# Kernel optimization log

Hardware: AMD Instinct MI355X
Metric: run time of the kernel (lower is better)

The kernel has to match this reference:

```python
import jax, jax.numpy as jnp
import numpy as np

N = 16384

def setup_inputs() -> dict:
    key = jax.random.key(0)
    k1, k2 = jax.random.split(key)
    inputs = jax.random.normal(k1, (N,), dtype=jnp.float32)
    targets = jax.random.randint(k2, (N,), 0, 2)  # int, values in {0,1}
    return {"inputs": inputs, "targets": targets}

def reference(inputs, targets):
    # Flatten, split logits into positives (targets==1) and negatives (targets==0).
    x = inputs.reshape(-1)
    t = targets.reshape(-1).astype(jnp.float32)
    pos_mask = (t == 1.0).astype(x.dtype)  # (N,)
    neg_mask = (t == 0.0).astype(x.dtype)  # (N,)
    # BCE-with-logits against target=1 on diff = x_i - x_j is softplus(-diff).
    # Masked full NxN formulation (jit-friendly, same math as pos/neg outer diff).
    diff = x[:, None] - x[None, :]                      # (N, N)
    pair_w = pos_mask[:, None] * neg_mask[None, :]      # 1 for (pos, neg) pairs
    loss_sum = jnp.sum(jax.nn.softplus(-diff) * pair_w)
    n_pairs = jnp.sum(pair_w)
    # Original returns 0.0 if no pos or no neg examples.
    return jnp.where(n_pairs > 0, loss_sum / jnp.maximum(n_pairs, 1.0), 0.0)
```

## Files before the change

### kernel.cpp

```cpp
#include <hip/hip_runtime.h>


#define CB   1024
#define PT2  512
#define RB   16
#define NW   (PT2 / 64)

__global__ __launch_bounds__(CB)
void compact_kernel(const float* __restrict__ x, const int* __restrict__ tg,
                    int n, float* __restrict__ pos_emp, float* __restrict__ neg_en,
                    int* __restrict__ cnts) {
    __shared__ float sbuf[16384];
    __shared__ int swsum[16], swoff[16], stot;
    const int tid  = threadIdx.x;
    const int lane = tid & 63, wid = tid >> 6;
    const int n4 = n >> 2;

    float4 vf[4]; int4 vt[4];
    int lp = 0, ln = 0;
#pragma unroll
    for (int k = 0; k < 4; ++k) {
        const int i4 = tid + k * CB;
        if (i4 < n4) { vf[k] = ((const float4*)x)[i4]; vt[k] = ((const int4*)tg)[i4]; }
        else         { vf[k] = make_float4(0,0,0,0); vt[k] = make_int4(-1,-1,-1,-1); }
        lp += (vt[k].x==1) + (vt[k].y==1) + (vt[k].z==1) + (vt[k].w==1);
        ln += (vt[k].x==0) + (vt[k].y==0) + (vt[k].z==0) + (vt[k].w==0);
    }

    const int c = lp | (ln << 16);
    int inc = c;
#pragma unroll
    for (int off = 1; off < 64; off <<= 1) {
        int u = __shfl_up(inc, off, 64);
        if (lane >= off) inc += u;
    }
    if (lane == 63) swsum[wid] = inc;
    __syncthreads();
    if (tid < 16) {
        int val = swsum[tid];
        int sc = val;
#pragma unroll
        for (int off = 1; off < 16; off <<= 1) {
            int u = __shfl_up(sc, off, 64);
            if (tid >= off) sc += u;
        }
        swoff[tid] = sc - val;
        if (tid == 15) stot = sc;
    }
    __syncthreads();
    const int ex = swoff[wid] + (inc - c);
    int op = ex & 0xffff;
    int on = ex >> 16;
#pragma unroll
    for (int k = 0; k < 4; ++k) {
        const float vx[4] = {vf[k].x, vf[k].y, vf[k].z, vf[k].w};
        const int   tx[4] = {vt[k].x, vt[k].y, vt[k].z, vt[k].w};
#pragma unroll
        for (int j = 0; j < 4; ++j) {
            if (tx[j] == 1)      sbuf[op++]           = __expf(-vx[j]);
            else if (tx[j] == 0) sbuf[n - 1 - (on++)] = __expf(vx[j]);
        }
    }
    __syncthreads();
    const int np = stot & 0xffff;
    const int nn = stot >> 16;
    const int nn_pad = (nn + 3) & ~3;
    for (int i = tid; i < np; i += CB)          pos_emp[i] = sbuf[i];
    for (int i = tid; i < nn; i += CB)          neg_en[i]  = sbuf[n - 1 - i];
    for (int i = nn + tid; i < nn_pad; i += CB) neg_en[i]  = 0.f;
    if (tid == 0) { cnts[0] = np; cnts[1] = nn; cnts[2] = nn_pad; }
}

__global__ __launch_bounds__(PT2)
void pair_kernel(const float* __restrict__ pos_emp, const float* __restrict__ neg_en,
                 const int* __restrict__ cnts, double* __restrict__ wpart) {
    const int bid = blockIdx.x, tid = threadIdx.x;
    const int wid = tid >> 6, lane = tid & 63;
    const int gw  = bid * NW + wid;
    const int np = cnts[0];
    const int nnpad4 = cnts[2] >> 2;
    const int rbase = bid * RB;

    if (rbase >= np || nnpad4 == 0) {
        if (lane == 0) wpart[gw] = 0.0;
        return;
    }

    float emp[RB];
#pragma unroll
    for (int r = 0; r < RB; ++r) {
        const int row = rbase + r;
        emp[r] = (row < np) ? pos_emp[row] : 0.f;
    }

    float acc0 = 0.f, acc1 = 0.f;
#define TERM(EN, R)  __builtin_fmaf((EN), emp[R], 1.0f)
#define Q4(EN, R0)   (((TERM(EN,R0) * TERM(EN,(R0)+1)) * TERM(EN,(R0)+2)) * TERM(EN,(R0)+3))
#define DO_COL(EN)                                      \
    do {                                                \
        const float en_ = (EN);                         \
        acc0 += __log2f(Q4(en_, 0) * Q4(en_, 4));       \
        acc1 += __log2f(Q4(en_, 8) * Q4(en_, 12));      \
    } while (0)

    const float4* __restrict__ en4 = (const float4*)neg_en;
#pragma unroll 2
    for (int v4 = tid; v4 < nnpad4; v4 += PT2) {
        const float4 e4 = en4[v4];
        DO_COL(e4.x);
        DO_COL(e4.y);
        DO_COL(e4.z);
        DO_COL(e4.w);
    }
#undef DO_COL
#undef Q4
#undef TERM

    float s = acc0 + acc1;
#pragma unroll
    for (int off = 32; off > 0; off >>= 1) s += __shfl_down(s, off, 64);
    if (lane == 0) wpart[gw] = (double)s;
}

__global__ __launch_bounds__(1024)
void finalize_kernel(const int* __restrict__ cnts, const double* __restrict__ wpart,
                     int nwaves, float* __restrict__ out) {
    const int tid = threadIdx.x;
    double d = 0.0;
    for (int k = tid; k < nwaves; k += 1024) d += wpart[k];
#pragma unroll
    for (int off = 32; off > 0; off >>= 1) d += __shfl_down(d, off, 64);
    __shared__ double fsum[16];
    if ((tid & 63) == 0) fsum[tid >> 6] = d;
    __syncthreads();
    if (tid == 0) {
        double s = 0.0;
#pragma unroll
        for (int w = 0; w < 16; ++w) s += fsum[w];
        const double npairs = (double)cnts[0] * (double)cnts[1];
        out[0] = (npairs > 0.0) ? (float)(s * 0.6931471805599453 / npairs) : 0.0f;
    }
}

extern "C" void kernel_launch(void* const* d_in, const int* in_sizes, int n_in,
                              void* d_out, int out_size, void* d_ws, size_t ws_size,
                              hipStream_t stream) {
    const float* x  = (const float*)d_in[0];
    const int*   tg = (const int*)d_in[1];
    const int n = in_sizes[0];

    char* ws = (char*)d_ws;
    float*  pos_emp = (float*)(ws);
    float*  neg_en  = (float*)(ws + 65536);
    int*    cnts    = (int*)(ws + 135168);
    double* wpart   = (double*)(ws + 139264);

    const int nblocks = (n + RB - 1) / RB;
    const int nwaves  = nblocks * NW;
    compact_kernel<<<1, CB, 0, stream>>>(x, tg, n, pos_emp, neg_en, cnts);
    pair_kernel<<<nblocks, PT2, 0, stream>>>(pos_emp, neg_en, cnts, wpart);
    finalize_kernel<<<1, 1024, 0, stream>>>(cnts, wpart, nwaves, (float*)d_out);
}
```

Measured before the change: 21.66 us.

## Parallelize compaction across 64 blocks with per-block prefix recount and ballot scatter

```diff
diff --git a/kernel.cpp b/kernel.cpp
--- a/kernel.cpp
+++ b/kernel.cpp
@@ -1,74 +1,74 @@
 #include <hip/hip_runtime.h>
 
 
-#define CB   1024
+#define K1B  64
+#define K1T  256
 #define PT2  512
 #define RB   16
 #define NW   (PT2 / 64)
 
-__global__ __launch_bounds__(CB)
-void compact_kernel(const float* __restrict__ x, const int* __restrict__ tg,
-                    int n, float* __restrict__ pos_emp, float* __restrict__ neg_en,
-                    int* __restrict__ cnts) {
-    __shared__ float sbuf[16384];
-    __shared__ int swsum[16], swoff[16], stot;
-    const int tid  = threadIdx.x;
-    const int lane = tid & 63, wid = tid >> 6;
-    const int n4 = n >> 2;
+__global__ __launch_bounds__(K1T)
+void pcompact(const float* __restrict__ x, const int* __restrict__ tg, int n,
+              float* __restrict__ pos_emp, float* __restrict__ neg_en,
+              int* __restrict__ cnts) {
+    __shared__ int wred[K1T / 64], wvc[K1T / 64], base_s, tots;
+    const int b = blockIdx.x, t = threadIdx.x;
+    const int lane = t & 63, w = t >> 6;
+    const int s0 = b * K1T;
 
-    float4 vf[4]; int4 vt[4];
-    int lp = 0, ln = 0;
+    int cp = 0, cn = 0;
+    const int4* t4 = (const int4*)tg;
+    for (int v = t; v < (s0 >> 2); v += K1T) {
+        const int4 tv = t4[v];
+        cp += (tv.x == 1) + (tv.y == 1) + (tv.z == 1) + (tv.w == 1);
+        cn += (tv.x == 0) + (tv.y == 0) + (tv.z == 0) + (tv.w == 0);
+    }
+    int pk = cp | (cn << 16);
 #pragma unroll
-    for (int k = 0; k < 4; ++k) {
-        const int i4 = tid + k * CB;
-        if (i4 < n4) { vf[k] = ((const float4*)x)[i4]; vt[k] = ((const int4*)tg)[i4]; }
-        else         { vf[k] = make_float4(0,0,0,0); vt[k] = make_int4(-1,-1,-1,-1); }
-        lp += (vt[k].x==1) + (vt[k].y==1) + (vt[k].z==1) + (vt[k].w==1);
-        ln += (vt[k].x==0) + (vt[k].y==0) + (vt[k].z==0) + (vt[k].w==0);
+    for (int off = 32; off > 0; off >>= 1) pk += __shfl_down(pk, off, 64);
+    if (lane == 0) wred[w] = pk;
+    __syncthreads();
+    if (t == 0) {
+        int s = 0;
+#pragma unroll
+        for (int i = 0; i < K1T / 64; ++i) s += wred[i];
+        base_s = s;
     }
 
-    const int c = lp | (ln << 16);
-    int inc = c;
+    const int e = s0 + t;
+    const int   tv = (e < n) ? tg[e] : -1;
+    const float xv = (e < n) ? x[e] : 0.f;
+    const int isp = (tv == 1), isn = (tv == 0);
+    const unsigned long long mp = __ballot(isp);
+    const unsigned long long mn = __ballot(isn);
+    if (lane == 0) wvc[w] = (int)__popcll(mp) | ((int)__popcll(mn) << 16);
+    __syncthreads();
+    int pre = 0;
+    for (int i = 0; i < w; ++i) pre += wvc[i];
+    const unsigned long long ltm = (1ull << lane) - 1ull;
+    if (isp) {
+        const int idx = (base_s & 0xffff) + (pre & 0xffff) + (int)__popcll(mp & ltm);
+        pos_emp[idx] = __expf(-xv);
+    } else if (isn) {
+        const int idx = ((base_s >> 16) & 0xffff) + ((pre >> 16) & 0xffff)
+                        + (int)__popcll(mn & ltm);
+        neg_en[idx] = __expf(xv);
+    }
+
+    if (b == K1B - 1) {
+        __syncthreads();
+        if (t == 0) {
+            int s = base_s;
 #pragma unroll
-    for (int off = 1; off < 64; off <<= 1) {
-        int u = __shfl_up(inc, off, 64);
-        if (lane >= off) inc += u;
+            for (int i = 0; i < K1T / 64; ++i) s += wvc[i];
+            tots = s;
+        }
+        __syncthreads();
+        const int np = tots & 0xffff, nn = (tots >> 16) & 0xffff;
+        const int nn_pad = (nn + 3) & ~3;
+        for (int i = nn + t; i < nn_pad; i += K1T) neg_en[i] = 0.f;
+        if (t == 0) { cnts[0] = np; cnts[1] = nn; cnts[2] = nn_pad; }
     }
-    if (lane == 63) swsum[wid] = inc;
-    __syncthreads();
-    if (tid < 16) {
-        int val = swsum[tid];
-        int sc = val;
-#pragma unroll
-        for (int off = 1; off < 16; off <<= 1) {
-            int u = __shfl_up(sc, off, 64);
-            if (tid >= off) sc += u;
-        }
-        swoff[tid] = sc - val;
-        if (tid == 15) stot = sc;
-    }
-    __syncthreads();
-    const int ex = swoff[wid] + (inc - c);
-    int op = ex & 0xffff;
-    int on = ex >> 16;
-#pragma unroll
-    for (int k = 0; k < 4; ++k) {
-        const float vx[4] = {vf[k].x, vf[k].y, vf[k].z, vf[k].w};
-        const int   tx[4] = {vt[k].x, vt[k].y, vt[k].z, vt[k].w};
-#pragma unroll
-        for (int j = 0; j < 4; ++j) {
-            if (tx[j] == 1)      sbuf[op++]           = __expf(-vx[j]);
-            else if (tx[j] == 0) sbuf[n - 1 - (on++)] = __expf(vx[j]);
-        }
-    }
-    __syncthreads();
-    const int np = stot & 0xffff;
-    const int nn = stot >> 16;
-    const int nn_pad = (nn + 3) & ~3;
-    for (int i = tid; i < np; i += CB)          pos_emp[i] = sbuf[i];
-    for (int i = tid; i < nn; i += CB)          neg_en[i]  = sbuf[n - 1 - i];
-    for (int i = nn + tid; i < nn_pad; i += CB) neg_en[i]  = 0.f;
-    if (tid == 0) { cnts[0] = np; cnts[1] = nn; cnts[2] = nn_pad; }
 }
 
 __global__ __launch_bounds__(PT2)
@@ -157,7 +157,7 @@
 
     const int nblocks = (n + RB - 1) / RB;
     const int nwaves  = nblocks * NW;
-    compact_kernel<<<1, CB, 0, stream>>>(x, tg, n, pos_emp, neg_en, cnts);
+    pcompact<<<K1B, K1T, 0, stream>>>(x, tg, n, pos_emp, neg_en, cnts);
     pair_kernel<<<nblocks, PT2, 0, stream>>>(pos_emp, neg_en, cnts, wpart);
     finalize_kernel<<<1, 1024, 0, stream>>>(cnts, wpart, nwaves, (float*)d_out);
 }
```

Result: faster. 20.25 us (-6.5%).
